# Kernel optimization log

Hardware: AMD Instinct MI355X
Metric: run time of the kernel (lower is better)

Reference implementation:

```python
import jax, jax.numpy as jnp
import numpy as np

H = 5      # hidden_size
P = 1      # proj_size
L = 50     # num_layers
G = 4 * H  # gate dim = 20


def _run_dir(x_tbi, Wih, Whh, bih, bhh, Whr, reverse):
    """One direction of one LSTM layer. x_tbi: [T, B, in]. Returns [T, B, P]."""
    Bn = x_tbi.shape[1]
    h0 = jnp.zeros((Bn, P), x_tbi.dtype)
    c0 = jnp.zeros((Bn, H), x_tbi.dtype)
    # precompute input contribution for all timesteps: [T, B, 4H]
    pre = jnp.einsum('tbi,gi->tbg', x_tbi, Wih) + bih + bhh

    def step(carry, px):
        h, c = carry
        g = px + h @ Whh.T                     # [B, 4H]
        i, f, gg, o = jnp.split(g, 4, axis=-1)  # PyTorch gate order i,f,g,o
        i = jax.nn.sigmoid(i)
        f = jax.nn.sigmoid(f)
        gg = jnp.tanh(gg)
        o = jax.nn.sigmoid(o)
        c = f * c + i * gg
        h = (o * jnp.tanh(c)) @ Whr.T          # projection to proj_size=1
        return (h, c), h

    _, hs = jax.lax.scan(step, (h0, c0), pre, reverse=reverse)
    return hs  # [T, B, P] (reverse=True yields outputs aligned to original time order, like torch)


def _forward(x, W_ih0, W_ih_rest, W_hh, b_ih, b_hh, W_hr):
    B = x.shape[0]
    inp = x.reshape(B, -1, 1).transpose(1, 0, 2)  # [T, B, 1]
    for layer in range(L):
        Wih_f = W_ih0[0] if layer == 0 else W_ih_rest[layer - 1, 0]
        Wih_b = W_ih0[1] if layer == 0 else W_ih_rest[layer - 1, 1]
        fwd = _run_dir(inp, Wih_f, W_hh[layer, 0], b_ih[layer, 0], b_hh[layer, 0], W_hr[layer, 0], False)
        bwd = _run_dir(inp, Wih_b, W_hh[layer, 1], b_ih[layer, 1], b_hh[layer, 1], W_hr[layer, 1], True)
        inp = jnp.concatenate([fwd, bwd], axis=-1)  # [T, B, 2]
    out = inp.transpose(1, 0, 2)      # [B, T, 2]
    ss = out.sum(axis=2)              # [B, T]
    stacked = jnp.stack((ss, 1.0 - ss), axis=1)  # [B, 2, T]
    return jax.nn.softmax(stacked, axis=1)


def setup_inputs() -> dict:
    key = jax.random.key(0)
    ks = jax.random.split(key, 7)
    B, T = 16, 8192
    s = 1.0 / np.sqrt(H)  # matches torch LSTM init scale
    return {
        'x': jax.random.normal(ks[0], (B, T), dtype=jnp.float32),
        'W_ih0': jax.random.normal(ks[1], (2, G, 1), dtype=jnp.float32) * s,
        'W_ih_rest': jax.random.normal(ks[2], (L - 1, 2, G, 2), dtype=jnp.float32) * s,
        'W_hh': jax.random.normal(ks[3], (L, 2, G, P), dtype=jnp.float32) * s,
        'b_ih': jax.random.normal(ks[4], (L, 2, G), dtype=jnp.float32) * s,
        'b_hh': jax.random.normal(ks[5], (L, 2, G), dtype=jnp.float32) * s,
        'W_hr': jax.random.normal(ks[6], (L, 2, P, H), dtype=jnp.float32) * s,
    }


def reference(x, W_ih0, W_ih_rest, W_hh, b_ih, b_hh, W_hr):
    return _forward(x, W_ih0, W_ih_rest, W_hh, b_ih, b_hh, W_hr)
```

## Files before the change

kernel.cpp:

```cpp
#include <hip/hip_runtime.h>

#define T_LEN 8192
#define BATCH 16
#define NLAYERS 50
#define NBLOCKS 256
#define CHUNK 32
#define WARM  16
#define BT (T_LEN * BATCH)
#define TOTW 49

static constexpr float kL = 1.44269504088896340736f;

template<int CTL>
__device__ __forceinline__ float dpp_f(float x) {
  return __int_as_float(__builtin_amdgcn_update_dpp(
      0, __float_as_int(x), CTL, 0xF, 0xF, true));
}

struct Wset { float wF[4], wB[4], bs[4], wh[4], whr; };

__global__ __launch_bounds__(256, 2) void lstm_main(
    const float* __restrict__ x,
    const float* __restrict__ W_ih0, const float* __restrict__ W_ih_rest,
    const float* __restrict__ W_hh, const float* __restrict__ b_ih,
    const float* __restrict__ b_hh, const float* __restrict__ W_hr,
    float* __restrict__ buf0, float* __restrict__ buf1,
    int* __restrict__ flags) {
  const int tid   = threadIdx.x;
  const int u     = tid & 7;
  const int g     = (tid & 63) >> 3;
  const int widx  = tid >> 6;
  const int ln    = tid & 63;
  const int c     = blockIdx.x;
  const int chain = widx * 8 + g;
  const int dir   = chain >> 4;
  const int b     = chain & 15;
  const bool act  = (u < 5);

  __shared__ float2 sIn[32 * TOTW];
  __shared__ float  hArr[2][16][33];
  float2* my = sIn + (tid >> 3) * TOTW;

  const int cs = c * CHUNK;
  int tstart, warm, dt;
  if (dir == 0) {
    int s0i = cs - WARM; s0i = s0i < 0 ? 0 : s0i;
    tstart = s0i; warm = cs - s0i; dt = 1;
  } else {
    int hi = cs + CHUNK - 1 + WARM; hi = hi > T_LEN - 1 ? T_LEN - 1 : hi;
    tstart = hi; warm = hi - (cs + CHUNK - 1); dt = -1;
  }
  const int total = warm + CHUNK;

  const int ebl = (widx & 1) * 8 + (ln >> 3);
  const int ej  = ln & 7;

  auto loadW = [&](int l) {
    Wset W{};
    if (act) {
      const int base = (l * 2 + dir) * 20;
#pragma unroll
      for (int gI = 0; gI < 4; ++gI) {
        const float s = (gI == 2) ? (-2.f * kL) : (-kL);
        const int k = gI * 5 + u;
        if (l == 0) {
          W.wF[gI] = W_ih0[dir * 20 + k] * s;  W.wB[gI] = 0.f;
        } else {
          const float* p = W_ih_rest + ((l - 1) * 2 + dir) * 40 + 2 * k;
          W.wF[gI] = p[0] * s;  W.wB[gI] = p[1] * s;
        }
        W.wh[gI] = W_hh[base + k] * s;
        W.bs[gI] = (b_ih[base + k] + b_hh[base + k]) * s;
      }
      W.whr = W_hr[(l * 2 + dir) * 5 + u];
    }
    return W;
  };

  Wset cw = loadW(0);

  for (int l = 0; l < NLAYERS; ++l) {
    if (l > 0) {
      for (int e = u; e < CHUNK; e += 8) {
        int hj = dir ? (CHUNK - 1 - e) : e;
        my[warm + e] = make_float2(hArr[0][b][hj], hArr[1][b][hj]);
      }
      if (tid < 2) {
        int n = c + (tid ? 1 : -1);
        n = n < 0 ? 0 : (n > NBLOCKS - 1 ? NBLOCKS - 1 : n);
        while (__hip_atomic_load(&flags[n << 4], __ATOMIC_RELAXED,
                                 __HIP_MEMORY_SCOPE_AGENT) < l)
          __builtin_amdgcn_s_sleep(1);
      }
      __syncthreads();
      const float* ib  = (l & 1) ? buf1 : buf0;
      const float* inF = ib;
      const float* inB = ib + BT;
      for (int e = u; e < warm; e += 8) {
        int o = b * T_LEN + (tstart + dt * e);
        float vf = __hip_atomic_load(inF + o, __ATOMIC_RELAXED, __HIP_MEMORY_SCOPE_AGENT);
        float vb = __hip_atomic_load(inB + o, __ATOMIC_RELAXED, __HIP_MEMORY_SCOPE_AGENT);
        my[e] = make_float2(vf, vb);
      }
    } else {
      for (int e = u; e < TOTW; e += 8) {
        int jj = e < total ? e : total - 1;
        float vf = x[b * T_LEN + (tstart + dt * jj)];
        my[e] = make_float2(vf, vf);
      }
      __syncthreads();
    }

    float C = 0.f, h = 0.f;
    int jh = dir ? (CHUNK - 1) : 0;

    auto step = [&](float2 in, bool st) {
      float g0 = __builtin_fmaf(h, cw.wh[0], __builtin_fmaf(in.y, cw.wB[0], __builtin_fmaf(in.x, cw.wF[0], cw.bs[0])));
      float g1 = __builtin_fmaf(h, cw.wh[1], __builtin_fmaf(in.y, cw.wB[1], __builtin_fmaf(in.x, cw.wF[1], cw.bs[1])));
      float g2 = __builtin_fmaf(h, cw.wh[2], __builtin_fmaf(in.y, cw.wB[2], __builtin_fmaf(in.x, cw.wF[2], cw.bs[2])));
      float g3 = __builtin_fmaf(h, cw.wh[3], __builtin_fmaf(in.y, cw.wB[3], __builtin_fmaf(in.x, cw.wF[3], cw.bs[3])));
      float e0 = __builtin_amdgcn_exp2f(g0);
      float e1 = __builtin_amdgcn_exp2f(g1);
      float e2 = __builtin_amdgcn_exp2f(g2);
      float e3 = __builtin_amdgcn_exp2f(g3);
      float a1  = 1.f + e1;
      float d02 = (1.f + e0) * (1.f + e2);
      float R   = __builtin_amdgcn_rcpf(d02 * a1);
      float num = __builtin_fmaf(e2, 2.f * kL, -2.f * kL);
      C = R * __builtin_fmaf(d02, C, num * a1);
      float ec = __builtin_amdgcn_exp2f(C);
      float rD = __builtin_amdgcn_rcpf((1.f + e3) * (1.f + ec));
      float y  = (cw.whr * (1.f - ec)) * rD;
      y += dpp_f<0x141>(y);
      y += dpp_f<0x1B>(y);
      y += dpp_f<0xB1>(y);
      h = y;
      if (st) {
        if (u == 0) hArr[dir][b][jh] = h;
        jh += dt;
      }
    };

    float2 cur = my[0];
    int i = 0;
    for (; i < warm; ++i) { float2 nx = my[i + 1]; step(cur, false); cur = nx; }
    for (; i < total; ++i) { float2 nx = my[i + 1]; step(cur, true); cur = nx; }

    if (l != NLAYERS - 1) {
      float* outp = (l & 1) ? buf0 : buf1;
      float* o = outp + dir * BT + ebl * T_LEN + cs;
      __hip_atomic_store(o + ej,      hArr[dir][ebl][ej],
                         __ATOMIC_RELAXED, __HIP_MEMORY_SCOPE_AGENT);
      __hip_atomic_store(o + ej + 8,  hArr[dir][ebl][ej + 8],
                         __ATOMIC_RELAXED, __HIP_MEMORY_SCOPE_AGENT);
      __hip_atomic_store(o + ej + 16, hArr[dir][ebl][ej + 16],
                         __ATOMIC_RELAXED, __HIP_MEMORY_SCOPE_AGENT);
      __hip_atomic_store(o + ej + 24, hArr[dir][ebl][ej + 24],
                         __ATOMIC_RELAXED, __HIP_MEMORY_SCOPE_AGENT);
    }

    __builtin_amdgcn_s_waitcnt(0);
    __syncthreads();
    if (tid == 0)
      __hip_atomic_store(&flags[c << 4], l + 1, __ATOMIC_RELAXED,
                         __HIP_MEMORY_SCOPE_AGENT);
    cw = loadW(l + 1 < NLAYERS ? l + 1 : l);
  }

  if (tid < 2) {
    int n = c + (tid ? 1 : -1);
    n = n < 0 ? 0 : (n > NBLOCKS - 1 ? NBLOCKS - 1 : n);
    while (__hip_atomic_load(&flags[n << 4], __ATOMIC_RELAXED,
                             __HIP_MEMORY_SCOPE_AGENT) < NLAYERS)
      __builtin_amdgcn_s_sleep(1);
  }
  __syncthreads();
  {
    int bb = tid >> 4, j0 = (tid & 15) * 2;
    float* out = buf1;
#pragma unroll
    for (int q = 0; q < 2; ++q) {
      int j = j0 + q;
      float ss = hArr[0][bb][j] + hArr[1][bb][j];
      float p = __builtin_amdgcn_rcpf(1.f + __builtin_amdgcn_exp2f((1.f - 2.f * ss) * kL));
      __hip_atomic_store(out + bb * (2 * T_LEN) + cs + j, p,
                         __ATOMIC_RELAXED, __HIP_MEMORY_SCOPE_AGENT);
      __hip_atomic_store(out + bb * (2 * T_LEN) + T_LEN + cs + j, 1.f - p,
                         __ATOMIC_RELAXED, __HIP_MEMORY_SCOPE_AGENT);
    }
  }
}

extern "C" void kernel_launch(void* const* d_in, const int* in_sizes, int n_in,
                              void* d_out, int out_size, void* d_ws, size_t ws_size,
                              hipStream_t stream) {
  const float* x         = (const float*)d_in[0];
  const float* W_ih0     = (const float*)d_in[1];
  const float* W_ih_rest = (const float*)d_in[2];
  const float* W_hh      = (const float*)d_in[3];
  const float* b_ih      = (const float*)d_in[4];
  const float* b_hh      = (const float*)d_in[5];
  const float* W_hr      = (const float*)d_in[6];
  float* out = (float*)d_out;

  int*   flags = (int*)d_ws;
  float* buf0  = (float*)((char*)d_ws + 32768);
  float* buf1  = out;

  lstm_main<<<NBLOCKS, 256, 0, stream>>>(x, W_ih0, W_ih_rest, W_hh, b_ih, b_hh,
                                         W_hr, buf0, buf1, flags);
}
```

Measured before the change: 494.1 us.

## Split each chunk into two interleaved half-chunk recurrences with shorter warmup

Each thread group now runs two independent LSTM recurrences in lockstep: one covers the first 16 timesteps of the chunk (with a 16-step warmup from the neighbour chunk) and the other covers the last 16, using the first half as its warmup. This halves the serial dependency chain per layer from 48 to 32 steps and interleaves two independent chains to hide transcendental latency. The second half's warmup now comes from the first half's inputs rather than its carried state, which changes the approximation and may affect accuracy. It also reshapes the gate algebra to use fmas.

Result: slower. 553.7 us (+12.1%).

```diff
diff --git a/kernel.cpp b/kernel.cpp
--- a/kernel.cpp
+++ b/kernel.cpp
@@ -4,10 +4,7 @@
 #define BATCH 16
 #define NLAYERS 50
 #define NBLOCKS 256
-#define CHUNK 32
-#define WARM  16
 #define BT (T_LEN * BATCH)
-#define TOTW 49
 
 static constexpr float kL = 1.44269504088896340736f;
 
@@ -37,20 +34,15 @@
   const int b     = chain & 15;
   const bool act  = (u < 5);
 
-  __shared__ float2 sIn[32 * TOTW];
+  __shared__ __attribute__((aligned(16))) float2 sIn[64 * 33];
   __shared__ float  hArr[2][16][33];
-  float2* my = sIn + (tid >> 3) * TOTW;
-
-  const int cs = c * CHUNK;
-  int tstart, warm, dt;
-  if (dir == 0) {
-    int s0i = cs - WARM; s0i = s0i < 0 ? 0 : s0i;
-    tstart = s0i; warm = cs - s0i; dt = 1;
-  } else {
-    int hi = cs + CHUNK - 1 + WARM; hi = hi > T_LEN - 1 ? T_LEN - 1 : hi;
-    tstart = hi; warm = hi - (cs + CHUNK - 1); dt = -1;
-  }
-  const int total = warm + CHUNK;
+  float2* myA = sIn + (tid >> 3) * 66;
+  float2* myB = myA + 33;
+
+  const int cs = c * 32;
+  int wExt, i0A, i0B;
+  if (dir == 0) { wExt = (c == 0) ? 0 : 16;           i0A = 16 - wExt; i0B = 0; }
+  else          { wExt = (c == NBLOCKS - 1) ? 0 : 16; i0B = 16 - wExt; i0A = 0; }
 
   const int ebl = (widx & 1) * 8 + (ln >> 3);
   const int ej  = ln & 7;
@@ -79,11 +71,21 @@
 
   Wset cw = loadW(0);
 
+#pragma unroll 1
   for (int l = 0; l < NLAYERS; ++l) {
     if (l > 0) {
-      for (int e = u; e < CHUNK; e += 8) {
-        int hj = dir ? (CHUNK - 1 - e) : e;
-        my[warm + e] = make_float2(hArr[0][b][hj], hArr[1][b][hj]);
+      for (int e = u; e < 16; e += 8) {
+        int jA = dir ? (15 - e) : e;
+        int jB = dir ? (31 - e) : (16 + e);
+        myA[16 + e] = make_float2(hArr[0][b][jA], hArr[1][b][jA]);
+        myB[16 + e] = make_float2(hArr[0][b][jB], hArr[1][b][jB]);
+      }
+      {
+        float2* myI = dir ? myA : myB;
+        for (int e = u; e < 16; e += 8) {
+          int j = dir ? (31 - e) : e;
+          myI[e] = make_float2(hArr[0][b][j], hArr[1][b][j]);
+        }
       }
       if (tid < 2) {
         int n = c + (tid ? 1 : -1);
@@ -93,58 +95,84 @@
           __builtin_amdgcn_s_sleep(1);
       }
       __syncthreads();
-      const float* ib  = (l & 1) ? buf1 : buf0;
-      const float* inF = ib;
-      const float* inB = ib + BT;
-      for (int e = u; e < warm; e += 8) {
-        int o = b * T_LEN + (tstart + dt * e);
-        float vf = __hip_atomic_load(inF + o, __ATOMIC_RELAXED, __HIP_MEMORY_SCOPE_AGENT);
-        float vb = __hip_atomic_load(inB + o, __ATOMIC_RELAXED, __HIP_MEMORY_SCOPE_AGENT);
-        my[e] = make_float2(vf, vb);
+      if (wExt) {
+        const float* ib  = (l & 1) ? buf1 : buf0;
+        const float* inF = ib;
+        const float* inB2 = ib + BT;
+        float2* myE = dir ? myB : myA;
+        for (int e = u; e < 16; e += 8) {
+          int t = dir ? (cs + 47 - e) : (cs - 16 + e);
+          int o = b * T_LEN + t;
+          float vf = __hip_atomic_load(inF + o, __ATOMIC_RELAXED, __HIP_MEMORY_SCOPE_AGENT);
+          float vb = __hip_atomic_load(inB2 + o, __ATOMIC_RELAXED, __HIP_MEMORY_SCOPE_AGENT);
+          myE[e] = make_float2(vf, vb);
+        }
       }
     } else {
-      for (int e = u; e < TOTW; e += 8) {
-        int jj = e < total ? e : total - 1;
-        float vf = x[b * T_LEN + (tstart + dt * jj)];
-        my[e] = make_float2(vf, vf);
-      }
-      __syncthreads();
-    }
-
-    float C = 0.f, h = 0.f;
-    int jh = dir ? (CHUNK - 1) : 0;
-
-    auto step = [&](float2 in, bool st) {
-      float g0 = __builtin_fmaf(h, cw.wh[0], __builtin_fmaf(in.y, cw.wB[0], __builtin_fmaf(in.x, cw.wF[0], cw.bs[0])));
-      float g1 = __builtin_fmaf(h, cw.wh[1], __builtin_fmaf(in.y, cw.wB[1], __builtin_fmaf(in.x, cw.wF[1], cw.bs[1])));
-      float g2 = __builtin_fmaf(h, cw.wh[2], __builtin_fmaf(in.y, cw.wB[2], __builtin_fmaf(in.x, cw.wF[2], cw.bs[2])));
-      float g3 = __builtin_fmaf(h, cw.wh[3], __builtin_fmaf(in.y, cw.wB[3], __builtin_fmaf(in.x, cw.wF[3], cw.bs[3])));
-      float e0 = __builtin_amdgcn_exp2f(g0);
-      float e1 = __builtin_amdgcn_exp2f(g1);
-      float e2 = __builtin_amdgcn_exp2f(g2);
-      float e3 = __builtin_amdgcn_exp2f(g3);
-      float a1  = 1.f + e1;
-      float d02 = (1.f + e0) * (1.f + e2);
-      float R   = __builtin_amdgcn_rcpf(d02 * a1);
-      float num = __builtin_fmaf(e2, 2.f * kL, -2.f * kL);
-      C = R * __builtin_fmaf(d02, C, num * a1);
-      float ec = __builtin_amdgcn_exp2f(C);
-      float rD = __builtin_amdgcn_rcpf((1.f + e3) * (1.f + ec));
-      float y  = (cw.whr * (1.f - ec)) * rD;
-      y += dpp_f<0x141>(y);
-      y += dpp_f<0x1B>(y);
-      y += dpp_f<0xB1>(y);
-      h = y;
-      if (st) {
-        if (u == 0) hArr[dir][b][jh] = h;
-        jh += dt;
-      }
+      int tsA = dir ? (cs + 31) : (cs - wExt);
+      int tsB = dir ? (cs + 31 + wExt) : cs;
+      int dtt = dir ? -1 : 1;
+      for (int i = u; i < 32; i += 8) {
+        int eA = i - i0A; eA = eA < 0 ? 0 : eA;
+        int eB = i - i0B; eB = eB < 0 ? 0 : eB;
+        float va = x[b * T_LEN + (tsA + dtt * eA)];
+        float vb = x[b * T_LEN + (tsB + dtt * eB)];
+        myA[i] = make_float2(va, va);
+        myB[i] = make_float2(vb, vb);
+      }
+    }
+
+    float CA = 0.f, hA = 0.f, CB = 0.f, hB = 0.f;
+
+    auto pairstep = [&](float2 iA, float2 iB, bool aA, bool aB) {
+      float gA0 = __builtin_fmaf(hA, cw.wh[0], __builtin_fmaf(iA.y, cw.wB[0], __builtin_fmaf(iA.x, cw.wF[0], cw.bs[0])));
+      float gB0 = __builtin_fmaf(hB, cw.wh[0], __builtin_fmaf(iB.y, cw.wB[0], __builtin_fmaf(iB.x, cw.wF[0], cw.bs[0])));
+      float gA1 = __builtin_fmaf(hA, cw.wh[1], __builtin_fmaf(iA.y, cw.wB[1], __builtin_fmaf(iA.x, cw.wF[1], cw.bs[1])));
+      float gB1 = __builtin_fmaf(hB, cw.wh[1], __builtin_fmaf(iB.y, cw.wB[1], __builtin_fmaf(iB.x, cw.wF[1], cw.bs[1])));
+      float gA2 = __builtin_fmaf(hA, cw.wh[2], __builtin_fmaf(iA.y, cw.wB[2], __builtin_fmaf(iA.x, cw.wF[2], cw.bs[2])));
+      float gB2 = __builtin_fmaf(hB, cw.wh[2], __builtin_fmaf(iB.y, cw.wB[2], __builtin_fmaf(iB.x, cw.wF[2], cw.bs[2])));
+      float gA3 = __builtin_fmaf(hA, cw.wh[3], __builtin_fmaf(iA.y, cw.wB[3], __builtin_fmaf(iA.x, cw.wF[3], cw.bs[3])));
+      float gB3 = __builtin_fmaf(hB, cw.wh[3], __builtin_fmaf(iB.y, cw.wB[3], __builtin_fmaf(iB.x, cw.wF[3], cw.bs[3])));
+      float eA0 = __builtin_amdgcn_exp2f(gA0);  float eB0 = __builtin_amdgcn_exp2f(gB0);
+      float eA1 = __builtin_amdgcn_exp2f(gA1);  float eB1 = __builtin_amdgcn_exp2f(gB1);
+      float eA2 = __builtin_amdgcn_exp2f(gA2);  float eB2 = __builtin_amdgcn_exp2f(gB2);
+      float eA3 = __builtin_amdgcn_exp2f(gA3);  float eB3 = __builtin_amdgcn_exp2f(gB3);
+      float a1A = 1.f + eA1;                    float a1B = 1.f + eB1;
+      float d0A = __builtin_fmaf(eA0, eA2, eA0 + eA2 + 1.f);
+      float d0B = __builtin_fmaf(eB0, eB2, eB0 + eB2 + 1.f);
+      float RA  = __builtin_amdgcn_rcpf(d0A * a1A);
+      float RB  = __builtin_amdgcn_rcpf(d0B * a1B);
+      float nmA = __builtin_fmaf(eA2, 2.f * kL, -2.f * kL);
+      float nmB = __builtin_fmaf(eB2, 2.f * kL, -2.f * kL);
+      float CnA = RA * __builtin_fmaf(d0A, CA, nmA * a1A);
+      float CnB = RB * __builtin_fmaf(d0B, CB, nmB * a1B);
+      CA = aA ? CnA : CA;                       CB = aB ? CnB : CB;
+      float ecA = __builtin_amdgcn_exp2f(CA);   float ecB = __builtin_amdgcn_exp2f(CB);
+      float ddA = __builtin_fmaf(eA3, ecA, eA3 + ecA + 1.f);
+      float ddB = __builtin_fmaf(eB3, ecB, eB3 + ecB + 1.f);
+      float rDA = __builtin_amdgcn_rcpf(ddA);   float rDB = __builtin_amdgcn_rcpf(ddB);
+      float tA  = __builtin_fmaf(-cw.whr, ecA, cw.whr);
+      float tB  = __builtin_fmaf(-cw.whr, ecB, cw.whr);
+      float yA  = tA * rDA;                     float yB  = tB * rDB;
+      yA += dpp_f<0x141>(yA);                   yB += dpp_f<0x141>(yB);
+      yA += dpp_f<0x1B>(yA);                    yB += dpp_f<0x1B>(yB);
+      yA += dpp_f<0xB1>(yA);                    yB += dpp_f<0xB1>(yB);
+      hA = aA ? yA : hA;                        hB = aB ? yB : hB;
     };
 
-    float2 cur = my[0];
-    int i = 0;
-    for (; i < warm; ++i) { float2 nx = my[i + 1]; step(cur, false); cur = nx; }
-    for (; i < total; ++i) { float2 nx = my[i + 1]; step(cur, true); cur = nx; }
+#pragma unroll 4
+    for (int i = 0; i < 16; ++i)
+      pairstep(myA[i], myB[i], i >= i0A, i >= i0B);
+#pragma unroll 4
+    for (int i = 16; i < 32; ++i) {
+      pairstep(myA[i], myB[i], true, true);
+      if (u == 0) {
+        int jA = dir ? (31 - i) : (i - 16);
+        int jB = dir ? (47 - i) : i;
+        hArr[dir][b][jA] = hA;
+        hArr[dir][b][jB] = hB;
+      }
+    }
 
     if (l != NLAYERS - 1) {
       float* outp = (l & 1) ? buf0 : buf1;
```

## Give each thread a 4-step chunk with all 5 hidden units and boundary handshakes

Applied to the files above, without the earlier changes.

Each thread now runs one full chain on a 4-timestep chunk with a 16-step warmup and computes all five hidden units itself, so the per-step DPP cross-lane reduction goes away. Activations stay in shared memory across layers. Only block-boundary warmup values are exchanged through small global buffers, using per-wave flags and consumer acknowledgements instead of full-layer global writes and block-level neighbour waits. The trade-off is more redundant warmup compute (20 steps per 4 outputs), more registers at one block per CU, and a more intricate flag/ack protocol with deadlock or race risk.

New measurement: 703.1 us. +42.3%, slower.

```diff
diff --git a/kernel.cpp b/kernel.cpp
--- a/kernel.cpp
+++ b/kernel.cpp
@@ -4,189 +4,194 @@
 #define BATCH 16
 #define NLAYERS 50
 #define NBLOCKS 256
-#define CHUNK 32
-#define WARM  16
-#define BT (T_LEN * BATCH)
-#define TOTW 49
+#define CHUNK 4
+#define WARM 16
+#define NSTEPS 20
 
 static constexpr float kL = 1.44269504088896340736f;
 
-template<int CTL>
-__device__ __forceinline__ float dpp_f(float x) {
-  return __int_as_float(__builtin_amdgcn_update_dpp(
-      0, __float_as_int(x), CTL, 0xF, 0xF, true));
-}
-
-struct Wset { float wF[4], wB[4], bs[4], wh[4], whr; };
-
-__global__ __launch_bounds__(256, 2) void lstm_main(
+#define ALOAD(p)     __hip_atomic_load((p),  __ATOMIC_RELAXED, __HIP_MEMORY_SCOPE_AGENT)
+#define ASTORE(p, v) __hip_atomic_store((p), (v), __ATOMIC_RELAXED, __HIP_MEMORY_SCOPE_AGENT)
+
+__global__ __launch_bounds__(256, 1) void lstm_main(
     const float* __restrict__ x,
     const float* __restrict__ W_ih0, const float* __restrict__ W_ih_rest,
     const float* __restrict__ W_hh, const float* __restrict__ b_ih,
     const float* __restrict__ b_hh, const float* __restrict__ W_hr,
-    float* __restrict__ buf0, float* __restrict__ buf1,
-    int* __restrict__ flags) {
-  const int tid   = threadIdx.x;
-  const int u     = tid & 7;
-  const int g     = (tid & 63) >> 3;
-  const int widx  = tid >> 6;
-  const int ln    = tid & 63;
-  const int c     = blockIdx.x;
-  const int chain = widx * 8 + g;
-  const int dir   = chain >> 4;
-  const int b     = chain & 15;
-  const bool act  = (u < 5);
-
-  __shared__ float2 sIn[32 * TOTW];
-  __shared__ float  hArr[2][16][33];
-  float2* my = sIn + (tid >> 3) * TOTW;
-
-  const int cs = c * CHUNK;
-  int tstart, warm, dt;
-  if (dir == 0) {
-    int s0i = cs - WARM; s0i = s0i < 0 ? 0 : s0i;
-    tstart = s0i; warm = cs - s0i; dt = 1;
-  } else {
-    int hi = cs + CHUNK - 1 + WARM; hi = hi > T_LEN - 1 ? T_LEN - 1 : hi;
-    tstart = hi; warm = hi - (cs + CHUNK - 1); dt = -1;
+    float* __restrict__ bnd, float* __restrict__ out,
+    int* __restrict__ gflag, int* __restrict__ cack) {
+  const int tid  = threadIdx.x;
+  const int widx = tid >> 6;
+  const int ln   = tid & 63;
+  const int b    = ln & 15;
+  const int slot = (ln >> 4) + 4 * (widx & 1);
+  const int c    = blockIdx.x;
+  const bool fwd = (widx < 2);
+  const int plane = fwd ? 0 : 1;
+  const int cs   = c * 32;
+  const int t0   = cs + CHUNK * slot;
+
+  __shared__ float hArr[2][32][17][2];
+
+  float* sA = bnd;
+  float* sB = bnd + 256 * 512;
+  float* pstr = nullptr;  bool hasCons = false;
+  if (widx == 0) { pstr = sB + c * 512 + 0;         hasCons = (c > 0);           }
+  if (widx == 2) { pstr = sB + c * 512 + 256;       hasCons = (c > 0);           }
+  if (widx == 1) { pstr = sA + (c + 1) * 512 + 0;   hasCons = (c < NBLOCKS - 1); }
+  if (widx == 3) { pstr = sA + (c + 1) * 512 + 256; hasCons = (c < NBLOCKS - 1); }
+  const bool consumer = (widx == 0 && c > 0) || (widx == 3 && c < NBLOCKS - 1);
+  const float* cstr = (widx == 0) ? (sA + c * 512) : (sB + (c + 1) * 512);
+  const int pf0 = (widx == 0) ? (((c - 1) << 4) | 1) : (((c + 1) << 4) | 0);
+  const int pf1 = (widx == 0) ? (((c - 1) << 4) | 3) : (((c + 1) << 4) | 2);
+  const int ackP = (widx == 0 || widx == 2) ? (((c - 1) << 4) | 3)
+                                            : (((c + 1) << 4) | 0);
+  const int ackC = (c << 4) | widx;
+
+  float wF[20], wB2[20], wh[20], bsv[20], whr[5];
+  auto loadW = [&](int l) {
+    const int base = (l * 2 + plane) * 20;
+#pragma unroll
+    for (int gI = 0; gI < 4; ++gI) {
+      const float s = (gI == 2) ? (-2.f * kL) : (-kL);
+#pragma unroll
+      for (int j = 0; j < 5; ++j) {
+        const int k = gI * 5 + j;
+        if (l == 0) { wF[k] = W_ih0[plane * 20 + k] * s; wB2[k] = 0.f; }
+        else {
+          const float* p = W_ih_rest + ((l - 1) * 2 + plane) * 40 + 2 * k;
+          wF[k] = p[0] * s; wB2[k] = p[1] * s;
+        }
+        wh[k]  = W_hh[base + k] * s;
+        bsv[k] = (b_ih[base + k] + b_hh[base + k]) * s;
+      }
+    }
+#pragma unroll
+    for (int j = 0; j < 5; ++j) whr[j] = W_hr[(l * 2 + plane) * 5 + j];
+  };
+  loadW(0);
+
+#pragma unroll 1
+  for (int l = 0; l < NLAYERS; ++l) {
+    const int pr = l & 1, rp = pr ^ 1;
+    float2 in[NSTEPS];
+
+    if (l == 0) {
+#pragma unroll
+      for (int k = 0; k < NSTEPS; ++k) {
+        int t = fwd ? (t0 - WARM + k) : (t0 + NSTEPS - 1 - k);
+        int tc = t < 0 ? 0 : (t > T_LEN - 1 ? T_LEN - 1 : t);
+        float v = x[b * T_LEN + tc];
+        in[k] = make_float2(v, v);
+      }
+    } else {
+      __syncthreads();
+#pragma unroll
+      for (int k = 0; k < NSTEPS; ++k) {
+        int t = fwd ? (t0 - WARM + k) : (t0 + NSTEPS - 1 - k);
+        int ti = t - cs;
+        bool inr = (ti >= 0) && (ti < 32);
+        int tc = inr ? ti : 0;
+        float2 v = *(const float2*)&hArr[rp][tc][b][0];
+        in[k] = inr ? v : make_float2(0.f, 0.f);
+      }
+      if (consumer) {
+        while (ALOAD(&gflag[pf0]) < l || ALOAD(&gflag[pf1]) < l)
+          __builtin_amdgcn_s_sleep(1);
+        asm volatile("" ::: "memory");
+        if (widx == 0) {
+          const int nneed = WARM - 4 * slot;
+#pragma unroll
+          for (int kk = 0; kk < WARM; ++kk) {
+            int ks = 4 * slot + kk; ks = ks > 15 ? 15 : ks;
+            float vF = ALOAD(cstr + ks * 16 + b);
+            float vB = ALOAD(cstr + 256 + ks * 16 + b);
+            if (kk < nneed) in[kk] = make_float2(vF, vB);
+          }
+        } else {
+          const int s2 = slot - 4;
+          const int nneed = 4 * s2 + 4;
+#pragma unroll
+          for (int kk = 0; kk < WARM; ++kk) {
+            int ks = 4 * s2 + 3 - kk; ks = ks < 0 ? 0 : ks;
+            float vF = ALOAD(cstr + ks * 16 + b);
+            float vB = ALOAD(cstr + 256 + ks * 16 + b);
+            if (kk < nneed) in[kk] = make_float2(vF, vB);
+          }
+        }
+        asm volatile("s_waitcnt vmcnt(0)" ::: "memory");
+        if (ln == 0) ASTORE(&cack[ackC], l);
+      }
+    }
+
+    float Cc[5] = {0.f, 0.f, 0.f, 0.f, 0.f};
+    float h = 0.f;
+    const bool pstore = hasCons && (l != NLAYERS - 1);
+
+    auto step = [&](float2 iv, bool on, bool st, int k) {
+      float hs = 0.f;
+#pragma unroll
+      for (int j = 0; j < 5; ++j) {
+        float g0 = __builtin_fmaf(h, wh[j],      __builtin_fmaf(iv.y, wB2[j],      __builtin_fmaf(iv.x, wF[j],      bsv[j])));
+        float g1 = __builtin_fmaf(h, wh[5 + j],  __builtin_fmaf(iv.y, wB2[5 + j],  __builtin_fmaf(iv.x, wF[5 + j],  bsv[5 + j])));
+        float g2 = __builtin_fmaf(h, wh[10 + j], __builtin_fmaf(iv.y, wB2[10 + j], __builtin_fmaf(iv.x, wF[10 + j], bsv[10 + j])));
+        float g3 = __builtin_fmaf(h, wh[15 + j], __builtin_fmaf(iv.y, wB2[15 + j], __builtin_fmaf(iv.x, wF[15 + j], bsv[15 + j])));
+        float e0 = __builtin_amdgcn_exp2f(g0);
+        float e1 = __builtin_amdgcn_exp2f(g1);
+        float e2 = __builtin_amdgcn_exp2f(g2);
+        float e3 = __builtin_amdgcn_exp2f(g3);
+        float a1  = 1.f + e1;
+        float d02 = __builtin_fmaf(e0, e2, e0 + e2 + 1.f);
+        float R   = __builtin_amdgcn_rcpf(d02 * a1);
+        float num = __builtin_fmaf(e2, 2.f * kL, -2.f * kL);
+        float Cn  = R * __builtin_fmaf(d02, Cc[j], num * a1);
+        Cc[j] = on ? Cn : Cc[j];
+        float ec = __builtin_amdgcn_exp2f(Cn);
+        float dd = __builtin_fmaf(e3, ec, e3 + ec + 1.f);
+        float rD = __builtin_amdgcn_rcpf(dd);
+        float we = __builtin_fmaf(-whr[j], ec, whr[j]);
+        hs = __builtin_fmaf(we, rD, hs);
+      }
+      h = on ? hs : h;
+      if (st) {
+        int ti = fwd ? (4 * slot + (k - WARM)) : (4 * slot + (NSTEPS - 1 - k));
+        hArr[pr][ti][b][plane] = h;
+        if (pstore) {
+          int kst = ti - ((widx & 1) << 4);
+          ASTORE(pstr + kst * 16 + b, h);
+        }
+      }
+    };
+
+#pragma unroll
+    for (int k = 0; k < WARM; ++k) {
+      int t = fwd ? (t0 - WARM + k) : (t0 + NSTEPS - 1 - k);
+      bool on = fwd ? (t >= 0) : (t <= T_LEN - 1);
+      step(in[k], on, false, k);
+    }
+    if (pstore && l > 0) {
+      while (ALOAD(&cack[ackP]) < l) __builtin_amdgcn_s_sleep(1);
+      asm volatile("" ::: "memory");
+    }
+#pragma unroll
+    for (int k = WARM; k < NSTEPS; ++k) step(in[k], true, true, k);
+
+    asm volatile("s_waitcnt vmcnt(0)" ::: "memory");
+    if (ln == 0 && l < NLAYERS - 1)
+      ASTORE(&gflag[(c << 4) | widx], l + 1);
+    loadW(l + 1 < NLAYERS ? l + 1 : l);
   }
-  const int total = warm + CHUNK;
-
-  const int ebl = (widx & 1) * 8 + (ln >> 3);
-  const int ej  = ln & 7;
-
-  auto loadW = [&](int l) {
-    Wset W{};
-    if (act) {
-      const int base = (l * 2 + dir) * 20;
-#pragma unroll
-      for (int gI = 0; gI < 4; ++gI) {
-        const float s = (gI == 2) ? (-2.f * kL) : (-kL);
-        const int k = gI * 5 + u;
-        if (l == 0) {
-          W.wF[gI] = W_ih0[dir * 20 + k] * s;  W.wB[gI] = 0.f;
-        } else {
-          const float* p = W_ih_rest + ((l - 1) * 2 + dir) * 40 + 2 * k;
-          W.wF[gI] = p[0] * s;  W.wB[gI] = p[1] * s;
-        }
-        W.wh[gI] = W_hh[base + k] * s;
-        W.bs[gI] = (b_ih[base + k] + b_hh[base + k]) * s;
-      }
-      W.whr = W_hr[(l * 2 + dir) * 5 + u];
-    }
-    return W;
-  };
-
-  Wset cw = loadW(0);
-
-  for (int l = 0; l < NLAYERS; ++l) {
-    if (l > 0) {
-      for (int e = u; e < CHUNK; e += 8) {
-        int hj = dir ? (CHUNK - 1 - e) : e;
-        my[warm + e] = make_float2(hArr[0][b][hj], hArr[1][b][hj]);
-      }
-      if (tid < 2) {
-        int n = c + (tid ? 1 : -1);
-        n = n < 0 ? 0 : (n > NBLOCKS - 1 ? NBLOCKS - 1 : n);
-        while (__hip_atomic_load(&flags[n << 4], __ATOMIC_RELAXED,
-                                 __HIP_MEMORY_SCOPE_AGENT) < l)
-          __builtin_amdgcn_s_sleep(1);
-      }
-      __syncthreads();
-      const float* ib  = (l & 1) ? buf1 : buf0;
-      const float* inF = ib;
-      const float* inB = ib + BT;
-      for (int e = u; e < warm; e += 8) {
-        int o = b * T_LEN + (tstart + dt * e);
-        float vf = __hip_atomic_load(inF + o, __ATOMIC_RELAXED, __HIP_MEMORY_SCOPE_AGENT);
-        float vb = __hip_atomic_load(inB + o, __ATOMIC_RELAXED, __HIP_MEMORY_SCOPE_AGENT);
-        my[e] = make_float2(vf, vb);
-      }
-    } else {
-      for (int e = u; e < TOTW; e += 8) {
-        int jj = e < total ? e : total - 1;
-        float vf = x[b * T_LEN + (tstart + dt * jj)];
-        my[e] = make_float2(vf, vf);
-      }
-      __syncthreads();
-    }
-
-    float C = 0.f, h = 0.f;
-    int jh = dir ? (CHUNK - 1) : 0;
-
-    auto step = [&](float2 in, bool st) {
-      float g0 = __builtin_fmaf(h, cw.wh[0], __builtin_fmaf(in.y, cw.wB[0], __builtin_fmaf(in.x, cw.wF[0], cw.bs[0])));
-      float g1 = __builtin_fmaf(h, cw.wh[1], __builtin_fmaf(in.y, cw.wB[1], __builtin_fmaf(in.x, cw.wF[1], cw.bs[1])));
-      float g2 = __builtin_fmaf(h, cw.wh[2], __builtin_fmaf(in.y, cw.wB[2], __builtin_fmaf(in.x, cw.wF[2], cw.bs[2])));
-      float g3 = __builtin_fmaf(h, cw.wh[3], __builtin_fmaf(in.y, cw.wB[3], __builtin_fmaf(in.x, cw.wF[3], cw.bs[3])));
-      float e0 = __builtin_amdgcn_exp2f(g0);
-      float e1 = __builtin_amdgcn_exp2f(g1);
-      float e2 = __builtin_amdgcn_exp2f(g2);
-      float e3 = __builtin_amdgcn_exp2f(g3);
-      float a1  = 1.f + e1;
-      float d02 = (1.f + e0) * (1.f + e2);
-      float R   = __builtin_amdgcn_rcpf(d02 * a1);
-      float num = __builtin_fmaf(e2, 2.f * kL, -2.f * kL);
-      C = R * __builtin_fmaf(d02, C, num * a1);
-      float ec = __builtin_amdgcn_exp2f(C);
-      float rD = __builtin_amdgcn_rcpf((1.f + e3) * (1.f + ec));
-      float y  = (cw.whr * (1.f - ec)) * rD;
-      y += dpp_f<0x141>(y);
-      y += dpp_f<0x1B>(y);
-      y += dpp_f<0xB1>(y);
-      h = y;
-      if (st) {
-        if (u == 0) hArr[dir][b][jh] = h;
-        jh += dt;
-      }
-    };
-
-    float2 cur = my[0];
-    int i = 0;
-    for (; i < warm; ++i) { float2 nx = my[i + 1]; step(cur, false); cur = nx; }
-    for (; i < total; ++i) { float2 nx = my[i + 1]; step(cur, true); cur = nx; }
-
-    if (l != NLAYERS - 1) {
-      float* outp = (l & 1) ? buf0 : buf1;
-      float* o = outp + dir * BT + ebl * T_LEN + cs;
-      __hip_atomic_store(o + ej,      hArr[dir][ebl][ej],
-                         __ATOMIC_RELAXED, __HIP_MEMORY_SCOPE_AGENT);
-      __hip_atomic_store(o + ej + 8,  hArr[dir][ebl][ej + 8],
-                         __ATOMIC_RELAXED, __HIP_MEMORY_SCOPE_AGENT);
-      __hip_atomic_store(o + ej + 16, hArr[dir][ebl][ej + 16],
-                         __ATOMIC_RELAXED, __HIP_MEMORY_SCOPE_AGENT);
-      __hip_atomic_store(o + ej + 24, hArr[dir][ebl][ej + 24],
-                         __ATOMIC_RELAXED, __HIP_MEMORY_SCOPE_AGENT);
-    }
-
-    __builtin_amdgcn_s_waitcnt(0);
-    __syncthreads();
-    if (tid == 0)
-      __hip_atomic_store(&flags[c << 4], l + 1, __ATOMIC_RELAXED,
-                         __HIP_MEMORY_SCOPE_AGENT);
-    cw = loadW(l + 1 < NLAYERS ? l + 1 : l);
-  }
-
-  if (tid < 2) {
-    int n = c + (tid ? 1 : -1);
-    n = n < 0 ? 0 : (n > NBLOCKS - 1 ? NBLOCKS - 1 : n);
-    while (__hip_atomic_load(&flags[n << 4], __ATOMIC_RELAXED,
-                             __HIP_MEMORY_SCOPE_AGENT) < NLAYERS)
-      __builtin_amdgcn_s_sleep(1);
-  }
+
   __syncthreads();
   {
-    int bb = tid >> 4, j0 = (tid & 15) * 2;
-    float* out = buf1;
+    int bb = tid >> 4, tI = (tid & 15) * 2;
 #pragma unroll
     for (int q = 0; q < 2; ++q) {
-      int j = j0 + q;
-      float ss = hArr[0][bb][j] + hArr[1][bb][j];
+      int ti = tI + q;
+      float ss = hArr[1][ti][bb][0] + hArr[1][ti][bb][1];
       float p = __builtin_amdgcn_rcpf(1.f + __builtin_amdgcn_exp2f((1.f - 2.f * ss) * kL));
-      __hip_atomic_store(out + bb * (2 * T_LEN) + cs + j, p,
-                         __ATOMIC_RELAXED, __HIP_MEMORY_SCOPE_AGENT);
-      __hip_atomic_store(out + bb * (2 * T_LEN) + T_LEN + cs + j, 1.f - p,
-                         __ATOMIC_RELAXED, __HIP_MEMORY_SCOPE_AGENT);
+      out[bb * (2 * T_LEN) + cs + ti] = p;
+      out[bb * (2 * T_LEN) + T_LEN + cs + ti] = 1.f - p;
     }
   }
 }
@@ -203,10 +208,10 @@
   const float* W_hr      = (const float*)d_in[6];
   float* out = (float*)d_out;
 
-  int*   flags = (int*)d_ws;
-  float* buf0  = (float*)((char*)d_ws + 32768);
-  float* buf1  = out;
+  int*   gflag = (int*)d_ws;
+  int*   cack  = (int*)d_ws + 4096;
+  float* bnd   = (float*)((char*)d_ws + 32768);
 
   lstm_main<<<NBLOCKS, 256, 0, stream>>>(x, W_ih0, W_ih_rest, W_hh, b_ih, b_hh,
-                                         W_hr, buf0, buf1, flags);
+                                         W_hr, bnd, out, gflag, cack);
 }
```
